# Kernel tuning notes

Measured on AMD Instinct MI355X. Metric: run time of the kernel, lower is better.

## Reference

```python
import jax, jax.numpy as jnp
import numpy as np

EPS_LN = 1e-5


def layer_norm(x, g, b):
    mu = jnp.mean(x, axis=-1, keepdims=True)
    var = jnp.mean((x - mu) ** 2, axis=-1, keepdims=True)
    return (x - mu) * jax.lax.rsqrt(var + EPS_LN) * g + b


def setup_inputs() -> dict:
    key = jax.random.key(0)
    ks = jax.random.split(key, 16)
    N, E, H, EA = 25000, 400000, 128, 1
    h = jax.random.normal(ks[0], (N, H), dtype=jnp.float32)
    coord = jax.random.normal(ks[1], (N, 3), dtype=jnp.float32)
    edge_index = jax.random.randint(ks[2], (2, E), 0, N, dtype=jnp.int64)
    edge_attr = jax.random.normal(ks[3], (E, EA), dtype=jnp.float32)

    def lin(k, fan_in, fan_out):
        lim = 1.0 / np.sqrt(fan_in)
        return jax.random.uniform(k, (fan_in, fan_out), jnp.float32, -lim, lim)

    in_edge = 2 * H + 1 + EA  # 258
    params = {
        'e_W1': lin(ks[4], in_edge, H), 'e_b1': jnp.zeros((H,), jnp.float32),
        'e_g1': jnp.ones((H,), jnp.float32), 'e_be1': jnp.zeros((H,), jnp.float32),
        'e_W2': lin(ks[5], H, H), 'e_b2': jnp.zeros((H,), jnp.float32),
        'e_g2': jnp.ones((H,), jnp.float32), 'e_be2': jnp.zeros((H,), jnp.float32),
        'n_W1': lin(ks[6], 2 * H, H), 'n_b1': jnp.zeros((H,), jnp.float32),
        'n_g1': jnp.ones((H,), jnp.float32), 'n_be1': jnp.zeros((H,), jnp.float32),
        'n_W2': lin(ks[7], H, H), 'n_b2': jnp.zeros((H,), jnp.float32),
        'c_W1': lin(ks[8], H, H), 'c_b1': jnp.zeros((H,), jnp.float32),
        'c_g1': jnp.ones((H,), jnp.float32), 'c_be1': jnp.zeros((H,), jnp.float32),
        # xavier_uniform with gain=0.001, no bias
        'c_W2': jax.random.uniform(ks[9], (H, 1), jnp.float32, -1.0, 1.0) * (0.001 * np.sqrt(6.0 / (H + 1))),
    }
    return dict(h=h, edge_index=edge_index, coord=coord, edge_attr=edge_attr, **params)


def reference(h, edge_index, coord, edge_attr,
              e_W1, e_b1, e_g1, e_be1, e_W2, e_b2, e_g2, e_be2,
              n_W1, n_b1, n_g1, n_be1, n_W2, n_b2,
              c_W1, c_b1, c_g1, c_be1, c_W2):
    N = h.shape[0]
    row, col = edge_index[0], edge_index[1]

    coord_diff = coord[row] - coord[col]                     # [E,3]
    radial = jnp.sum(coord_diff ** 2, axis=1, keepdims=True)  # [E,1]
    norm = jnp.sqrt(radial + 1e-8)
    coord_diff = coord_diff / (norm + 1.0)

    inp = jnp.concatenate([h[row], h[col], radial, edge_attr], axis=1)  # [E,258]
    x = jax.nn.silu(layer_norm(inp @ e_W1 + e_b1, e_g1, e_be1))
    edge_feat = jax.nn.silu(layer_norm(x @ e_W2 + e_b2, e_g2, e_be2))   # [E,H]

    cm = jax.nn.silu(layer_norm(edge_feat @ c_W1 + c_b1, c_g1, c_be1)) @ c_W2  # [E,1]
    trans = coord_diff * cm                                   # [E,3]

    coord_out = coord + jax.ops.segment_sum(trans, row, num_segments=N)
    agg = jax.ops.segment_sum(edge_feat, row, num_segments=N)  # [N,H]

    node_in = jnp.concatenate([h, agg], axis=1)               # [N,2H]
    out = jax.nn.silu(layer_norm(node_in @ n_W1 + n_b1, n_g1, n_be1)) @ n_W2 + n_b2
    out = h + out  # recurrent
    return out, coord_out
```

## Files before the change

kernel.cpp:

```cpp
#include <hip/hip_runtime.h>
#include <math.h>

#define H 128
#define KE 256
#define KN 256
#define XSTR 136
#define SSTR 132

typedef __attribute__((ext_vector_type(8))) short bf16x8;
typedef __attribute__((ext_vector_type(4))) float f32x4;

__device__ __forceinline__ float silu_f(float x) { return x / (1.0f + __expf(-x)); }

__device__ __forceinline__ unsigned short f2bf(float f) {
    unsigned int u = __float_as_uint(f);
    unsigned int r = u + 0x7FFFu + ((u >> 16) & 1u);
    return (unsigned short)(r >> 16);
}

__device__ __forceinline__ unsigned int pkbf(float a, float b) {
#if defined(__has_builtin)
#if __has_builtin(__builtin_amdgcn_cvt_pk_bf16_f32)
    typedef __attribute__((ext_vector_type(2))) __bf16 bf16x2_t;
    bf16x2_t v = __builtin_amdgcn_cvt_pk_bf16_f32(a, b);
    return *(unsigned int*)&v;
#else
    return (unsigned int)f2bf(a) | ((unsigned int)f2bf(b) << 16);
#endif
#else
    return (unsigned int)f2bf(a) | ((unsigned int)f2bf(b) << 16);
#endif
}

__device__ __forceinline__ float bflo(unsigned int w) { return __uint_as_float(w << 16); }
__device__ __forceinline__ float bfhi(unsigned int w) { return __uint_as_float(w & 0xFFFF0000u); }

__device__ __forceinline__ void atomic_pk_add_bf16(unsigned short* addr, unsigned int pkv) {
    asm volatile("global_atomic_pk_add_bf16 %0, %1, off"
                 :: "v"(addr), "v"(pkv) : "memory");
}

template<int CTRL>
__device__ __forceinline__ float dpp_add(float x) {
    int t = __builtin_amdgcn_update_dpp(0, __float_as_int(x), CTRL, 0xF, 0xF, true);
    return x + __int_as_float(t);
}
__device__ __forceinline__ float red16(float x) {
    x = dpp_add<0x128>(x);
    x = dpp_add<0x124>(x);
    x = dpp_add<0x122>(x);
    x = dpp_add<0x121>(x);
    return x;
}

__device__ __forceinline__ void wfrag(const float* __restrict__ W,
                                      unsigned short* __restrict__ Wf, int f) {
    int kb = f >> 9, rem = f & 511;
    int nt = rem >> 6, lane = rem & 63;
    int quad = lane >> 4, l15 = lane & 15;
    int n = nt * 16 + l15, k0 = kb * 32 + quad * 8;
    union { bf16x8 v; unsigned short u[8]; } pk;
    #pragma unroll
    for (int j = 0; j < 8; ++j) pk.u[j] = f2bf(W[(size_t)(k0 + j) * H + n]);
    *(bf16x8*)&Wf[(size_t)f * 8] = pk.v;
}

__global__ __launch_bounds__(256) void prep_all(
    const float* __restrict__ h, unsigned short* __restrict__ hb, int n4_h,
    float* __restrict__ aggz, int n4_agg,
    const float* __restrict__ coord, float* __restrict__ coord_out, int n_coord,
    const float* __restrict__ eW1, const float* __restrict__ eW2,
    const float* __restrict__ cW1, const float* __restrict__ nW1,
    const float* __restrict__ nW2,
    unsigned short* __restrict__ eW1f, unsigned short* __restrict__ eW2f,
    unsigned short* __restrict__ cW1f, unsigned short* __restrict__ nW1f,
    unsigned short* __restrict__ nW2f,
    int b0, int b1, int b2)
{
    int b = blockIdx.x;
    int t = threadIdx.x;
    if (b < b0) {
        int i = b * 256 + t;
        if (i < n4_h) {
            float4 f = ((const float4*)h)[i];
            ((uint2*)hb)[i] = make_uint2(pkbf(f.x, f.y), pkbf(f.z, f.w));
        }
    } else if (b < b1) {
        int i = (b - b0) * 256 + t;
        if (i < n4_agg) ((float4*)aggz)[i] = (float4){0.f, 0.f, 0.f, 0.f};
    } else if (b < b2) {
        int i = (b - b1) * 256 + t;
        if (i < n_coord) coord_out[i] = coord[i];
    } else {
        int idx = (b - b2) * 256 + t;
        if      (idx <  4096) wfrag(eW1, eW1f, idx);
        else if (idx <  8192) wfrag(nW1, nW1f, idx - 4096);
        else if (idx < 10240) wfrag(eW2, eW2f, idx - 8192);
        else if (idx < 12288) wfrag(cW1, cW1f, idx - 10240);
        else if (idx < 14336) wfrag(nW2, nW2f, idx - 12288);
    }
}

__global__ __launch_bounds__(256, 4) void proj_kernel(
    const unsigned short* __restrict__ hb,
    const unsigned short* __restrict__ eW1f,
    unsigned short* __restrict__ Pb, int N)
{
    __shared__ unsigned short Ys[4][16 * 256];

    const int wv = threadIdx.x >> 6;
    const int lane = threadIdx.x & 63;
    const int l15 = lane & 15, quad = lane >> 4;
    const int gn0 = (blockIdx.x * 4 + wv) * 16;
    unsigned short* Y = &Ys[wv][0];

    if (gn0 >= N) return;
    int nl = gn0 + l15; if (nl >= N) nl = N - 1;

    f32x4 a1[8], a2[8];
    #pragma unroll
    for (int nt = 0; nt < 8; ++nt) {
        a1[nt] = (f32x4){0.f, 0.f, 0.f, 0.f};
        a2[nt] = (f32x4){0.f, 0.f, 0.f, 0.f};
    }

    for (int kb = 0; kb < 4; ++kb) {
        int ko = kb * 32 + quad * 8;
        bf16x8 af = *(const bf16x8*)(hb + (size_t)nl * H + ko);
        const unsigned short* bp1 = eW1f + ((size_t)kb * 8) * 512 + (size_t)lane * 8;
        const unsigned short* bp2 = eW1f + ((size_t)(kb + 4) * 8) * 512 + (size_t)lane * 8;
        #pragma unroll
        for (int nt = 0; nt < 8; ++nt) {
            bf16x8 b1 = *(const bf16x8*)(bp1 + (size_t)nt * 512);
            bf16x8 b2 = *(const bf16x8*)(bp2 + (size_t)nt * 512);
            a1[nt] = __builtin_amdgcn_mfma_f32_16x16x32_bf16(af, b1, a1[nt], 0, 0, 0);
            a2[nt] = __builtin_amdgcn_mfma_f32_16x16x32_bf16(af, b2, a2[nt], 0, 0, 0);
        }
    }

    #pragma unroll
    for (int nt = 0; nt < 8; ++nt) {
        int c = nt * 16 + l15;
        #pragma unroll
        for (int r = 0; r < 4; ++r) {
            int rr = quad * 4 + r;
            Y[rr * 256 + c]       = f2bf(a1[nt][r]);
            Y[rr * 256 + 128 + c] = f2bf(a2[nt][r]);
        }
    }

    const int m = lane >> 2, part = lane & 3;
    int gm = gn0 + m; if (gm >= N) gm = N - 1;
    #pragma unroll
    for (int j = 0; j < 8; ++j) {
        uint4 v = *(const uint4*)&Y[m * 256 + part * 64 + j * 8];
        *(uint4*)(Pb + (size_t)gm * 256 + part * 64 + j * 8) = v;
    }
}

__device__ __forceinline__ void ln_silu_store1(
    f32x4* acc, const float* __restrict__ bias, const float* __restrict__ g,
    const float* __restrict__ be, unsigned short* X, int l15, int quad)
{
    float s[4] = {0,0,0,0}, q[4] = {0,0,0,0};
    #pragma unroll
    for (int nt = 0; nt < 8; ++nt) {
        float b = bias[nt * 16 + l15];
        #pragma unroll
        for (int r = 0; r < 4; ++r) {
            float x = acc[nt][r] + b; acc[nt][r] = x; s[r] += x; q[r] += x * x;
        }
    }
    #pragma unroll
    for (int r = 0; r < 4; ++r) { s[r] = red16(s[r]); q[r] = red16(q[r]); }
    #pragma unroll
    for (int r = 0; r < 4; ++r) {
        float mu = s[r] * 0.0078125f, v = q[r] * 0.0078125f - mu * mu;
        s[r] = mu; q[r] = rsqrtf(v + 1e-5f);
    }
    #pragma unroll
    for (int nt = 0; nt < 8; ++nt) {
        float gg = g[nt * 16 + l15], bb = be[nt * 16 + l15];
        #pragma unroll
        for (int r = 0; r < 4; ++r) {
            float a = q[r] * gg, c = bb - s[r] * a;
            float y = silu_f(fmaf(acc[nt][r], a, c));
            acc[nt][r] = y;
            X[(quad * 4 + r) * XSTR + nt * 16 + l15] = f2bf(y);
        }
    }
}

__global__ __launch_bounds__(64, 4) void edge_kernel(
    const unsigned short* __restrict__ Pb, const int* __restrict__ ei,
    const float* __restrict__ coord, const float* __restrict__ eattr,
    const float* __restrict__ eW1,
    const float* __restrict__ eb1, const float* __restrict__ eg1, const float* __restrict__ ebe1,
    const unsigned short* __restrict__ eW2f,
    const float* __restrict__ eb2, const float* __restrict__ eg2, const float* __restrict__ ebe2,
    const unsigned short* __restrict__ cW1f,
    const float* __restrict__ cb1, const float* __restrict__ cg1, const float* __restrict__ cbe1,
    const float* __restrict__ cW2,
    unsigned short* __restrict__ aggb, float* __restrict__ coord_out, int E)
{
    __shared__ float S[16 * SSTR];
    unsigned short* X = (unsigned short*)S;

    const int lane = threadIdx.x;
    const int l15 = lane & 15, quad = lane >> 4;
    const int ge0 = blockIdx.x * 16;

    int el  = ge0 + l15;
    int elc = (el < E) ? el : (E - 1);
    int rowl = ei[elc], coll = ei[E + elc];
    float dx = coord[rowl * 3 + 0] - coord[coll * 3 + 0];
    float dy = coord[rowl * 3 + 1] - coord[coll * 3 + 1];
    float dz = coord[rowl * 3 + 2] - coord[coll * 3 + 2];
    float radial = dx * dx + dy * dy + dz * dz;
    float inv = 1.0f / (sqrtf(radial + 1e-8f) + 1.0f);
    float cdx = dx * inv, cdy = dy * inv, cdz = dz * inv;
    float ea = eattr[elc];

    {
        const int m = lane >> 2, part = lane & 3;
        int row_m = __shfl(rowl, m, 64);
        int col_m = __shfl(coll, m, 64);
        const unsigned short* p1 = Pb + (size_t)row_m * 256 + part * 32;
        const unsigned short* p2 = Pb + (size_t)col_m * 256 + 128 + part * 32;
        #pragma unroll
        for (int j = 0; j < 4; ++j) {
            uint4 a = *(const uint4*)(p1 + j * 8);
            uint4 b = *(const uint4*)(p2 + j * 8);
            float4 v0, v1;
            v0.x = bflo(a.x) + bflo(b.x); v0.y = bfhi(a.x) + bfhi(b.x);
            v0.z = bflo(a.y) + bflo(b.y); v0.w = bfhi(a.y) + bfhi(b.y);
            v1.x = bflo(a.z) + bflo(b.z); v1.y = bfhi(a.z) + bfhi(b.z);
            v1.z = bflo(a.w) + bflo(b.w); v1.w = bfhi(a.w) + bfhi(b.w);
            *(float4*)&S[m * SSTR + part * 32 + j * 8]     = v0;
            *(float4*)&S[m * SSTR + part * 32 + j * 8 + 4] = v1;
        }
    }

    f32x4 acc[8];
    {
        float rad_r[4], ea_r[4];
        #pragma unroll
        for (int r = 0; r < 4; ++r) {
            rad_r[r] = __shfl(radial, quad * 4 + r, 64);
            ea_r[r]  = __shfl(ea,     quad * 4 + r, 64);
        }
        #pragma unroll
        for (int nt = 0; nt < 8; ++nt) {
            float w256 = eW1[256 * H + nt * 16 + l15];
            float w257 = eW1[257 * H + nt * 16 + l15];
            #pragma unroll
            for (int r = 0; r < 4; ++r) {
                float base = S[(quad * 4 + r) * SSTR + nt * 16 + l15];
                acc[nt][r] = base + rad_r[r] * w256 + ea_r[r] * w257;
            }
        }
    }

    ln_silu_store1(acc, eb1, eg1, ebe1, X, l15, quad);

    f32x4 ac2[8];
    #pragma unroll
    for (int nt = 0; nt < 8; ++nt) ac2[nt] = (f32x4){0.f, 0.f, 0.f, 0.f};
    for (int kb = 0; kb < 4; ++kb) {
        bf16x8 af = *(const bf16x8*)&X[l15 * XSTR + kb * 32 + quad * 8];
        const unsigned short* bp = eW2f + ((size_t)kb * 8) * 512 + (size_t)lane * 8;
        #pragma unroll
        for (int nt = 0; nt < 8; ++nt) {
            bf16x8 bf = *(const bf16x8*)(bp + (size_t)nt * 512);
            ac2[nt] = __builtin_amdgcn_mfma_f32_16x16x32_bf16(af, bf, ac2[nt], 0, 0, 0);
        }
    }

    ln_silu_store1(ac2, eb2, eg2, ebe2, X, l15, quad);

    {
        int rowm[4];
        #pragma unroll
        for (int r = 0; r < 4; ++r) rowm[r] = __shfl(rowl, quad * 4 + r, 64);
        #pragma unroll
        for (int c4 = 0; c4 < 4; ++c4) {
            #pragma unroll
            for (int r = 0; r < 4; ++r) {
                int geh = ge0 + quad * 4 + r;
                if (geh < E) {
                    unsigned int pkv =
                        *(const unsigned int*)&X[(quad * 4 + r) * XSTR + c4 * 32 + 2 * l15];
                    atomic_pk_add_bf16(aggb + (size_t)rowm[r] * H + c4 * 32 + 2 * l15, pkv);
                }
            }
        }
    }

    #pragma unroll
    for (int nt = 0; nt < 8; ++nt) acc[nt] = (f32x4){0.f, 0.f, 0.f, 0.f};
    for (int kb = 0; kb < 4; ++kb) {
        bf16x8 af = *(const bf16x8*)&X[l15 * XSTR + kb * 32 + quad * 8];
        const unsigned short* bp = cW1f + ((size_t)kb * 8) * 512 + (size_t)lane * 8;
        #pragma unroll
        for (int nt = 0; nt < 8; ++nt) {
            bf16x8 bf = *(const bf16x8*)(bp + (size_t)nt * 512);
            acc[nt] = __builtin_amdgcn_mfma_f32_16x16x32_bf16(af, bf, acc[nt], 0, 0, 0);
        }
    }

    {
        float s[4] = {0,0,0,0}, q[4] = {0,0,0,0};
        #pragma unroll
        for (int nt = 0; nt < 8; ++nt) {
            float b = cb1[nt * 16 + l15];
            #pragma unroll
            for (int r = 0; r < 4; ++r) {
                float x = acc[nt][r] + b; acc[nt][r] = x; s[r] += x; q[r] += x * x;
            }
        }
        #pragma unroll
        for (int r = 0; r < 4; ++r) { s[r] = red16(s[r]); q[r] = red16(q[r]); }
        #pragma unroll
        for (int r = 0; r < 4; ++r) {
            float mu = s[r] * 0.0078125f, v = q[r] * 0.0078125f - mu * mu;
            s[r] = mu; q[r] = rsqrtf(v + 1e-5f);
        }
        float cm[4] = {0,0,0,0};
        #pragma unroll
        for (int nt = 0; nt < 8; ++nt) {
            float gg = cg1[nt * 16 + l15], bb = cbe1[nt * 16 + l15];
            float w2 = cW2[nt * 16 + l15];
            #pragma unroll
            for (int r = 0; r < 4; ++r) {
                float a = q[r] * gg, c = bb - s[r] * a;
                cm[r] += silu_f(fmaf(acc[nt][r], a, c)) * w2;
            }
        }
        #pragma unroll
        for (int r = 0; r < 4; ++r) cm[r] = red16(cm[r]);
        #pragma unroll
        for (int r = 0; r < 4; ++r) {
            int src = quad * 4 + r;
            float cdxr = __shfl(cdx, src, 64);
            float cdyr = __shfl(cdy, src, 64);
            float cdzr = __shfl(cdz, src, 64);
            int rw = __shfl(rowl, src, 64);
            float comp = (l15 == 0) ? cdxr : ((l15 == 1) ? cdyr : cdzr);
            int geh = ge0 + src;
            if (l15 < 3 && geh < E)
                atomicAdd(&coord_out[(size_t)rw * 3 + l15], comp * cm[r]);
        }
    }
}

__global__ __launch_bounds__(256, 4) void node_kernel(
    const unsigned short* __restrict__ hb, const float* __restrict__ h,
    const unsigned short* __restrict__ aggb,
    const unsigned short* __restrict__ nW1f,
    const float* __restrict__ nb1, const float* __restrict__ ng1, const float* __restrict__ nbe1,
    const unsigned short* __restrict__ nW2f, const float* __restrict__ nb2,
    float* __restrict__ out, int N)
{
    __shared__ unsigned short Xs[4][16 * XSTR];

    const int wv   = threadIdx.x >> 6;
    const int lane = threadIdx.x & 63;
    const int l15 = lane & 15, quad = lane >> 4;
    const int gn0 = (blockIdx.x * 4 + wv) * 16;
    unsigned short* X = &Xs[wv][0];

    if (gn0 >= N) return;
    int nl = gn0 + l15; if (nl >= N) nl = N - 1;

    f32x4 acc[8];
    #pragma unroll
    for (int nt = 0; nt < 8; ++nt) acc[nt] = (f32x4){0.f, 0.f, 0.f, 0.f};

    for (int kb = 0; kb < 8; ++kb) {
        int ko = (kb & 3) * 32 + quad * 8;
        const unsigned short* src = (kb < 4) ? hb : aggb;
        bf16x8 af = *(const bf16x8*)(src + (size_t)nl * H + ko);
        const unsigned short* bp = nW1f + ((size_t)kb * 8) * 512 + (size_t)lane * 8;
        #pragma unroll
        for (int nt = 0; nt < 8; ++nt) {
            bf16x8 bf = *(const bf16x8*)(bp + (size_t)nt * 512);
            acc[nt] = __builtin_amdgcn_mfma_f32_16x16x32_bf16(af, bf, acc[nt], 0, 0, 0);
        }
    }

    ln_silu_store1(acc, nb1, ng1, nbe1, X, l15, quad);

    f32x4 ac2[8];
    #pragma unroll
    for (int nt = 0; nt < 8; ++nt) ac2[nt] = (f32x4){0.f, 0.f, 0.f, 0.f};
    for (int kb = 0; kb < 4; ++kb) {
        bf16x8 af = *(const bf16x8*)&X[l15 * XSTR + kb * 32 + quad * 8];
        const unsigned short* bp = nW2f + ((size_t)kb * 8) * 512 + (size_t)lane * 8;
        #pragma unroll
        for (int nt = 0; nt < 8; ++nt) {
            bf16x8 bf = *(const bf16x8*)(bp + (size_t)nt * 512);
            ac2[nt] = __builtin_amdgcn_mfma_f32_16x16x32_bf16(af, bf, ac2[nt], 0, 0, 0);
        }
    }

    #pragma unroll
    for (int nt = 0; nt < 8; ++nt) {
        float b = nb2[nt * 16 + l15];
        #pragma unroll
        for (int r = 0; r < 4; ++r) {
            int gn = gn0 + quad * 4 + r;
            if (gn < N) {
                size_t idx = (size_t)gn * H + nt * 16 + l15;
                out[idx] = ac2[nt][r] + b + h[idx];
            }
        }
    }
}

extern "C" void kernel_launch(void* const* d_in, const int* in_sizes, int n_in,
                              void* d_out, int out_size, void* d_ws, size_t ws_size,
                              hipStream_t stream) {
    const float* h     = (const float*)d_in[0];
    const int*   ei    = (const int*)d_in[1];
    const float* coord = (const float*)d_in[2];
    const float* eattr = (const float*)d_in[3];
    const float* eW1   = (const float*)d_in[4];
    const float* eb1   = (const float*)d_in[5];
    const float* eg1   = (const float*)d_in[6];
    const float* ebe1  = (const float*)d_in[7];
    const float* eW2   = (const float*)d_in[8];
    const float* eb2   = (const float*)d_in[9];
    const float* eg2   = (const float*)d_in[10];
    const float* ebe2  = (const float*)d_in[11];
    const float* nW1   = (const float*)d_in[12];
    const float* nb1   = (const float*)d_in[13];
    const float* ng1   = (const float*)d_in[14];
    const float* nbe1  = (const float*)d_in[15];
    const float* nW2   = (const float*)d_in[16];
    const float* nb2   = (const float*)d_in[17];
    const float* cW1   = (const float*)d_in[18];
    const float* cb1   = (const float*)d_in[19];
    const float* cg1   = (const float*)d_in[20];
    const float* cbe1  = (const float*)d_in[21];
    const float* cW2   = (const float*)d_in[22];

    const int N = in_sizes[0] / H;
    const int E = in_sizes[1] / 2;

    float* out       = (float*)d_out;
    float* coord_out = out + (size_t)N * H;

    char* ws = (char*)d_ws;
    size_t o = 0;
    unsigned short* aggb = (unsigned short*)(ws + o); o += (size_t)N * H * 2;
    unsigned short* hb   = (unsigned short*)(ws + o); o += (size_t)N * H * 2;
    unsigned short* Pb   = (unsigned short*)(ws + o); o += (size_t)N * 256 * 2;
    unsigned short* eW1f = (unsigned short*)(ws + o); o += (size_t)H * KE * 2;
    unsigned short* eW2f = (unsigned short*)(ws + o); o += (size_t)H * H * 2;
    unsigned short* cW1f = (unsigned short*)(ws + o); o += (size_t)H * H * 2;
    unsigned short* nW1f = (unsigned short*)(ws + o); o += (size_t)H * KN * 2;
    unsigned short* nW2f = (unsigned short*)(ws + o); o += (size_t)H * H * 2;

    const int n4_h   = N * H / 4;
    const int n4_agg = N * H / 8;
    const int n_co   = N * 3;
    const int b0 = (n4_h   + 255) / 256;
    const int b1 = b0 + (n4_agg + 255) / 256;
    const int b2 = b1 + (n_co   + 255) / 256;
    const int bw = (4096 + 4096 + 2048 + 2048 + 2048 + 255) / 256;
    prep_all<<<b2 + bw, 256, 0, stream>>>(
        h, hb, n4_h, (float*)aggb, n4_agg, coord, coord_out, n_co,
        eW1, eW2, cW1, nW1, nW2,
        eW1f, eW2f, cW1f, nW1f, nW2f, b0, b1, b2);

    proj_kernel<<<(N + 63) / 64, 256, 0, stream>>>(hb, eW1f, Pb, N);

    edge_kernel<<<(E + 15) / 16, 64, 0, stream>>>(
        Pb, ei, coord, eattr,
        eW1, eb1, eg1, ebe1,
        eW2f, eb2, eg2, ebe2,
        cW1f, cb1, cg1, cbe1, cW2,
        aggb, coord_out, E);

    node_kernel<<<(N + 63) / 64, 256, 0, stream>>>(
        hb, h, aggb, nW1f, nb1, ng1, nbe1, nW2f, nb2, out, N);
}
```

Baseline: 319.3 us.

## Store node projections in fp32 and fuse edge layer-1 LayerNorm into gather

The per-node projection buffer P is now stored as fp32 and written straight from MFMA accumulators, with no LDS staging or bf16 conversion. The edge kernel gathers P[row] and P[col] as float4, adds the radial, edge-attribute and bias terms, and computes the first LayerNorm+SiLU in the gather layout. The row statistics are reduced across 4 lanes with shuffles, and the result is written to LDS as packed bf16. This removes a round trip through LDS and the separate ln_silu pass, but doubles the bytes of the random per-edge gathers from P and of the P workspace.

New measurement: 397.7 us. 24.6% more time.

```diff
diff --git a/kernel.cpp b/kernel.cpp
--- a/kernel.cpp
+++ b/kernel.cpp
@@ -5,7 +5,6 @@
 #define KE 256
 #define KN 256
 #define XSTR 136
-#define SSTR 132
 
 typedef __attribute__((ext_vector_type(8))) short bf16x8;
 typedef __attribute__((ext_vector_type(4))) float f32x4;
@@ -31,9 +30,6 @@
     return (unsigned int)f2bf(a) | ((unsigned int)f2bf(b) << 16);
 #endif
 }
-
-__device__ __forceinline__ float bflo(unsigned int w) { return __uint_as_float(w << 16); }
-__device__ __forceinline__ float bfhi(unsigned int w) { return __uint_as_float(w & 0xFFFF0000u); }
 
 __device__ __forceinline__ void atomic_pk_add_bf16(unsigned short* addr, unsigned int pkv) {
     asm volatile("global_atomic_pk_add_bf16 %0, %1, off"
@@ -104,15 +100,12 @@
 __global__ __launch_bounds__(256, 4) void proj_kernel(
     const unsigned short* __restrict__ hb,
     const unsigned short* __restrict__ eW1f,
-    unsigned short* __restrict__ Pb, int N)
+    float* __restrict__ Pf, int N)
 {
-    __shared__ unsigned short Ys[4][16 * 256];
-
     const int wv = threadIdx.x >> 6;
     const int lane = threadIdx.x & 63;
     const int l15 = lane & 15, quad = lane >> 4;
     const int gn0 = (blockIdx.x * 4 + wv) * 16;
-    unsigned short* Y = &Ys[wv][0];
 
     if (gn0 >= N) return;
     int nl = gn0 + l15; if (nl >= N) nl = N - 1;
@@ -139,22 +132,16 @@
     }
 
     #pragma unroll
-    for (int nt = 0; nt < 8; ++nt) {
-        int c = nt * 16 + l15;
-        #pragma unroll
-        for (int r = 0; r < 4; ++r) {
-            int rr = quad * 4 + r;
-            Y[rr * 256 + c]       = f2bf(a1[nt][r]);
-            Y[rr * 256 + 128 + c] = f2bf(a2[nt][r]);
-        }
-    }
-
-    const int m = lane >> 2, part = lane & 3;
-    int gm = gn0 + m; if (gm >= N) gm = N - 1;
-    #pragma unroll
-    for (int j = 0; j < 8; ++j) {
-        uint4 v = *(const uint4*)&Y[m * 256 + part * 64 + j * 8];
-        *(uint4*)(Pb + (size_t)gm * 256 + part * 64 + j * 8) = v;
+    for (int r = 0; r < 4; ++r) {
+        int gn = gn0 + quad * 4 + r;
+        if (gn < N) {
+            float* dst = Pf + (size_t)gn * 256 + l15;
+            #pragma unroll
+            for (int nt = 0; nt < 8; ++nt) {
+                dst[nt * 16]       = a1[nt][r];
+                dst[128 + nt * 16] = a2[nt][r];
+            }
+        }
     }
 }
 
@@ -192,7 +179,7 @@
 }
 
 __global__ __launch_bounds__(64, 4) void edge_kernel(
-    const unsigned short* __restrict__ Pb, const int* __restrict__ ei,
+    const float* __restrict__ Pf, const int* __restrict__ ei,
     const float* __restrict__ coord, const float* __restrict__ eattr,
     const float* __restrict__ eW1,
     const float* __restrict__ eb1, const float* __restrict__ eg1, const float* __restrict__ ebe1,
@@ -203,8 +190,7 @@
     const float* __restrict__ cW2,
     unsigned short* __restrict__ aggb, float* __restrict__ coord_out, int E)
 {
-    __shared__ float S[16 * SSTR];
-    unsigned short* X = (unsigned short*)S;
+    __shared__ unsigned short X[16 * XSTR];
 
     const int lane = threadIdx.x;
     const int l15 = lane & 15, quad = lane >> 4;
@@ -223,45 +209,56 @@
 
     {
         const int m = lane >> 2, part = lane & 3;
-        int row_m = __shfl(rowl, m, 64);
-        int col_m = __shfl(coll, m, 64);
-        const unsigned short* p1 = Pb + (size_t)row_m * 256 + part * 32;
-        const unsigned short* p2 = Pb + (size_t)col_m * 256 + 128 + part * 32;
-        #pragma unroll
-        for (int j = 0; j < 4; ++j) {
-            uint4 a = *(const uint4*)(p1 + j * 8);
-            uint4 b = *(const uint4*)(p2 + j * 8);
-            float4 v0, v1;
-            v0.x = bflo(a.x) + bflo(b.x); v0.y = bfhi(a.x) + bfhi(b.x);
-            v0.z = bflo(a.y) + bflo(b.y); v0.w = bfhi(a.y) + bfhi(b.y);
-            v1.x = bflo(a.z) + bflo(b.z); v1.y = bfhi(a.z) + bfhi(b.z);
-            v1.z = bflo(a.w) + bflo(b.w); v1.w = bfhi(a.w) + bfhi(b.w);
-            *(float4*)&S[m * SSTR + part * 32 + j * 8]     = v0;
-            *(float4*)&S[m * SSTR + part * 32 + j * 8 + 4] = v1;
-        }
-    }
-
-    f32x4 acc[8];
-    {
-        float rad_r[4], ea_r[4];
-        #pragma unroll
-        for (int r = 0; r < 4; ++r) {
-            rad_r[r] = __shfl(radial, quad * 4 + r, 64);
-            ea_r[r]  = __shfl(ea,     quad * 4 + r, 64);
-        }
-        #pragma unroll
-        for (int nt = 0; nt < 8; ++nt) {
-            float w256 = eW1[256 * H + nt * 16 + l15];
-            float w257 = eW1[257 * H + nt * 16 + l15];
-            #pragma unroll
-            for (int r = 0; r < 4; ++r) {
-                float base = S[(quad * 4 + r) * SSTR + nt * 16 + l15];
-                acc[nt][r] = base + rad_r[r] * w256 + ea_r[r] * w257;
-            }
-        }
-    }
-
-    ln_silu_store1(acc, eb1, eg1, ebe1, X, l15, quad);
+        int   row_m = __shfl(rowl,   m, 64);
+        int   col_m = __shfl(coll,   m, 64);
+        float rad_m = __shfl(radial, m, 64);
+        float ea_m  = __shfl(ea,     m, 64);
+        const float4* p1 = (const float4*)(Pf + (size_t)row_m * 256 + part * 32);
+        const float4* p2 = (const float4*)(Pf + (size_t)col_m * 256 + 128 + part * 32);
+        const float4* w6 = (const float4*)(eW1 + 256 * H + part * 32);
+        const float4* w7 = (const float4*)(eW1 + 257 * H + part * 32);
+        const float4* bb = (const float4*)(eb1 + part * 32);
+
+        float4 v[8];
+        float s = 0.f, q = 0.f;
+        #pragma unroll
+        for (int j = 0; j < 8; ++j) {
+            float4 a = p1[j], b = p2[j];
+            float4 w6j = w6[j], w7j = w7[j], b4 = bb[j];
+            float4 t;
+            t.x = a.x + b.x + rad_m * w6j.x + ea_m * w7j.x + b4.x;
+            t.y = a.y + b.y + rad_m * w6j.y + ea_m * w7j.y + b4.y;
+            t.z = a.z + b.z + rad_m * w6j.z + ea_m * w7j.z + b4.z;
+            t.w = a.w + b.w + rad_m * w6j.w + ea_m * w7j.w + b4.w;
+            v[j] = t;
+            s += t.x + t.y + t.z + t.w;
+            q = fmaf(t.x, t.x, q); q = fmaf(t.y, t.y, q);
+            q = fmaf(t.z, t.z, q); q = fmaf(t.w, t.w, q);
+        }
+        s += __shfl_xor(s, 1, 64); q += __shfl_xor(q, 1, 64);
+        s += __shfl_xor(s, 2, 64); q += __shfl_xor(q, 2, 64);
+        float mu   = s * 0.0078125f;
+        float rstd = rsqrtf(q * 0.0078125f - mu * mu + 1e-5f);
+
+        const float4* gg = (const float4*)(eg1 + part * 32);
+        const float4* ee = (const float4*)(ebe1 + part * 32);
+        #pragma unroll
+        for (int j = 0; j < 8; j += 2) {
+            float4 g0 = gg[j], e0 = ee[j], g1 = gg[j + 1], e1 = ee[j + 1];
+            float y0 = silu_f(fmaf(v[j].x - mu,     g0.x * rstd, e0.x));
+            float y1 = silu_f(fmaf(v[j].y - mu,     g0.y * rstd, e0.y));
+            float y2 = silu_f(fmaf(v[j].z - mu,     g0.z * rstd, e0.z));
+            float y3 = silu_f(fmaf(v[j].w - mu,     g0.w * rstd, e0.w));
+            float y4 = silu_f(fmaf(v[j + 1].x - mu, g1.x * rstd, e1.x));
+            float y5 = silu_f(fmaf(v[j + 1].y - mu, g1.y * rstd, e1.y));
+            float y6 = silu_f(fmaf(v[j + 1].z - mu, g1.z * rstd, e1.z));
+            float y7 = silu_f(fmaf(v[j + 1].w - mu, g1.w * rstd, e1.w));
+            uint4 pk4;
+            pk4.x = pkbf(y0, y1); pk4.y = pkbf(y2, y3);
+            pk4.z = pkbf(y4, y5); pk4.w = pkbf(y6, y7);
+            *(uint4*)&X[m * XSTR + part * 32 + j * 4] = pk4;
+        }
+    }
 
     f32x4 ac2[8];
     #pragma unroll
@@ -296,6 +293,7 @@
         }
     }
 
+    f32x4 acc[8];
     #pragma unroll
     for (int nt = 0; nt < 8; ++nt) acc[nt] = (f32x4){0.f, 0.f, 0.f, 0.f};
     for (int kb = 0; kb < 4; ++kb) {
@@ -454,7 +452,7 @@
     size_t o = 0;
     unsigned short* aggb = (unsigned short*)(ws + o); o += (size_t)N * H * 2;
     unsigned short* hb   = (unsigned short*)(ws + o); o += (size_t)N * H * 2;
-    unsigned short* Pb   = (unsigned short*)(ws + o); o += (size_t)N * 256 * 2;
+    float*          Pf   = (float*)(ws + o);          o += (size_t)N * 256 * 4;
     unsigned short* eW1f = (unsigned short*)(ws + o); o += (size_t)H * KE * 2;
     unsigned short* eW2f = (unsigned short*)(ws + o); o += (size_t)H * H * 2;
     unsigned short* cW1f = (unsigned short*)(ws + o); o += (size_t)H * H * 2;
@@ -473,10 +471,10 @@
         eW1, eW2, cW1, nW1, nW2,
         eW1f, eW2f, cW1f, nW1f, nW2f, b0, b1, b2);
 
-    proj_kernel<<<(N + 63) / 64, 256, 0, stream>>>(hb, eW1f, Pb, N);
+    proj_kernel<<<(N + 63) / 64, 256, 0, stream>>>(hb, eW1f, Pf, N);
 
     edge_kernel<<<(E + 15) / 16, 64, 0, stream>>>(
-        Pb, ei, coord, eattr,
+        Pf, ei, coord, eattr,
         eW1, eb1, eg1, ebe1,
         eW2f, eb2, eg2, ebe2,
         cW1f, cb1, cg1, cbe1, cW2,
```
